# Kernel tuning notes

Hardware: AMD Instinct MI355X
Metric: run time of the kernel (lower is better)

The kernel has to match this reference:

```python
import jax, jax.numpy as jnp
import numpy as np


def _conv3x3_replicate(x, w, b):
    # replicate (edge) padding then VALID 3x3 conv, NCHW / OIHW
    x = jnp.pad(x, ((0, 0), (0, 0), (1, 1), (1, 1)), mode='edge')
    y = jax.lax.conv_general_dilated(
        x, w, window_strides=(1, 1), padding='VALID',
        dimension_numbers=('NCHW', 'OIHW', 'NCHW'))
    return y + b[None, :, None, None]


def setup_inputs() -> dict:
    key = jax.random.key(0)
    ks = jax.random.split(key, 9)
    B, Cin, H, W = 8, 3, 256, 256
    Q, NC, Cout = 64, 32, 64
    x = jax.random.normal(ks[0], (B, Cin, H, W), dtype=jnp.float32)
    # Convx2: two 3x3 convs (replicate padding), then a 1x1 conv
    w1 = jax.random.normal(ks[1], (Q, Cin, 3, 3), dtype=jnp.float32) * (1.0 / np.sqrt(Cin * 9))
    b1 = jnp.zeros((Q,), jnp.float32)
    w2 = jax.random.normal(ks[2], (Q, Q, 3, 3), dtype=jnp.float32) * (1.0 / np.sqrt(Q * 9))
    b2 = jnp.zeros((Q,), jnp.float32)
    w3 = jax.random.normal(ks[3], (Q, Q, 1, 1), dtype=jnp.float32) * (1.0 / np.sqrt(Q))
    b3 = jnp.zeros((Q,), jnp.float32)
    cluster_mu = jax.random.normal(ks[4], (1, NC, Q, 1, 1), dtype=jnp.float32)
    cluster_label = jax.random.normal(ks[5], (Cout, NC), dtype=jnp.float32)
    return {'x': x, 'w1': w1, 'b1': b1, 'w2': w2, 'b2': b2, 'w3': w3, 'b3': b3,
            'cluster_mu': cluster_mu, 'cluster_label': cluster_label}


def reference(x, w1, b1, w2, b2, w3, b3, cluster_mu, cluster_label):
    # query encoder: Convx2 (conv3x3 -> ReLU -> conv3x3 -> ReLU) + 1x1 conv
    q = jax.nn.relu(_conv3x3_replicate(x, w1, b1))
    q = jax.nn.relu(_conv3x3_replicate(q, w2, b2))
    Qd = w3.shape[0]
    q = jnp.einsum('bchw,oc->bohw', q, w3.reshape(Qd, Qd)) + b3[None, :, None, None]  # (B,Q,H,W)
    # squared-distance logits, expanded form: -(||q||^2 - 2 q.mu + ||mu||^2)
    mu = cluster_mu.reshape(cluster_mu.shape[1], cluster_mu.shape[2])  # (NC,Q)
    qn = jnp.sum(q * q, axis=1)                       # (B,H,W)
    dot = jnp.einsum('bqhw,nq->bnhw', q, mu)          # (B,NC,H,W)
    mun = jnp.sum(mu * mu, axis=1)                    # (NC,)
    logit = -(qn[:, None] - 2.0 * dot + mun[None, :, None, None])
    attention = jax.nn.softmax(logit, axis=1)         # (B,NC,H,W)
    res = jnp.einsum('on,bnhw->bohw', cluster_label, attention)
    return res
```

## Files before the change

kernel.cpp:

```cpp
#include <hip/hip_runtime.h>

typedef _Float16 f16x8 __attribute__((ext_vector_type(8)));
typedef __fp16   half2 __attribute__((ext_vector_type(2)));
typedef float    f32x4 __attribute__((ext_vector_type(4)));

#define H_ 256
#define W_ 256

#define WS_W1S 0
#define WS_W2S 4096
#define WS_STG 77824
#define STG_U4 520

#define L_SX   0
#define L_SQ1  4800
#define L_W2S  26304
#define L_STG  63168
#define L_SQ2  26304
#define L_PT   0
#define LDS_SZ 71488

__global__ void repack_kernel(const float* __restrict__ w1, const float* __restrict__ b1,
                              const float* __restrict__ w2, const float* __restrict__ w3,
                              const float* __restrict__ b3, const float* __restrict__ mu,
                              const float* __restrict__ label, char* __restrict__ ws)
{
    int t = blockIdx.x * 256 + threadIdx.x;
    _Float16* w1s  = (_Float16*)(ws + WS_W1S);
    _Float16* w2s  = (_Float16*)(ws + WS_W2S);
    _Float16* mws  = (_Float16*)(ws + WS_STG);
    _Float16* labs = (_Float16*)(ws + WS_STG + 4096);
    float*    tn   = (float*)(ws + WS_STG + 8192);

    if (t < 2048) {
        int o = t >> 5, k = t & 31;
        float v = (k < 27) ? w1[o * 27 + k] : ((k == 27) ? b1[o] : 0.f);
        w1s[o * 32 + k] = (_Float16)v;
    }
    if (t < 36864) {
        int n = t / 576, rem = t % 576, c = rem / 9, tap = rem % 9;
        int chunk = c >> 5, k = c & 31;
        int slot = (k >> 3) ^ ((n ^ (n >> 2)) & 3);
        w2s[((chunk * 9 + tap) * 64 + n) * 32 + slot * 8 + (k & 7)] = (_Float16)w2[t];
    }
    if (t < 2048) {
        int n = t >> 6, c = t & 63;
        float s = 0.f;
        for (int o = 0; o < 64; ++o) s += mu[n * 64 + o] * w3[o * 64 + c];
        int slot = (c >> 3) ^ (n & 7);
        mws[n * 64 + slot * 8 + (c & 7)] = (_Float16)s;
    }
    if (t < 2048) {
        int o = t >> 5, cl = t & 31;
        int slot = (cl >> 3) ^ ((o ^ (o >> 2)) & 3);
        labs[o * 32 + slot * 8 + (cl & 7)] = (_Float16)label[o * 32 + cl];
    }
    if (t < 32) {
        float d = 0.f, m2 = 0.f;
        for (int o = 0; o < 64; ++o) { float m = mu[t * 64 + o]; d += m * b3[o]; m2 += m * m; }
        tn[t] = 2.f * d - m2;
    }
}

__global__ __launch_bounds__(256, 2) void fused_kernel(
    const float* __restrict__ x, const char* __restrict__ ws,
    const float* __restrict__ b2, float* __restrict__ out)
{
    __shared__ __align__(16) char smem[LDS_SZ];
    const int tid = threadIdx.x;
    const int lane = tid & 63;
    const int wv = tid >> 6;
    const int ln = lane & 15;
    const int lg = lane >> 4;
    const int swl = (ln ^ (ln >> 2)) & 3;
    const int w0 = blockIdx.x * 16, h0 = blockIdx.y * 16, bz = blockIdx.z;

    {
        const uint4* s = (const uint4*)(ws + WS_STG);
        uint4* d = (uint4*)(smem + L_STG);
        for (int i = tid; i < STG_U4; i += 256) d[i] = s[i];
    }
    {
        const uint4* s = (const uint4*)(ws + WS_W2S);
        uint4* d = (uint4*)(smem + L_W2S);
        for (int i = tid; i < 2304; i += 256) d[i] = s[i];
    }
    {
        float* sx = (float*)(smem + L_SX);
        for (int i = tid; i < 1200; i += 256) {
            int ci = i / 400, r = (i / 20) % 20, c = i % 20;
            int gy = min(max(h0 - 2 + r, 0), H_ - 1);
            int gx = min(max(w0 - 2 + c, 0), W_ - 1);
            sx[i] = x[((bz * 3 + ci) * H_ + gy) * W_ + gx];
        }
    }
    float b2v[4][4];
#pragma unroll
    for (int nb = 0; nb < 4; ++nb)
#pragma unroll
        for (int jr = 0; jr < 4; ++jr)
            b2v[nb][jr] = b2[nb * 16 + lg * 4 + jr];

    int koff[8]; float kcv[8]; int kvalid[8];
#pragma unroll
    for (int j = 0; j < 8; ++j) {
        int k = lg * 8 + j;
        int ci = (k * 57) >> 9;
        int r  = k - 9 * ci;
        int dy = (r * 22) >> 6;
        int dx = r - 3 * dy;
        koff[j]   = ci * 400 + dy * 20 + dx;
        kvalid[j] = (k < 27);
        kcv[j]    = (k == 27) ? 1.0f : 0.0f;
    }

    __syncthreads();

    const f16x8* w1sp = (const f16x8*)(ws + WS_W1S);
    const float* sxp = (const float*)(smem + L_SX);

    f32x4 acc[4][4];
#pragma unroll
    for (int i = 0; i < 4; ++i)
#pragma unroll
        for (int nb = 0; nb < 4; ++nb)
            acc[i][nb] = (f32x4){b2v[nb][0], b2v[nb][1], b2v[nb][2], b2v[nb][3]};

    f16x8 bfr[6];
    int wrow[6], wswp[6];

    {
        f16x8 w1f[2];
#pragma unroll
        for (int nb2 = 0; nb2 < 2; ++nb2)
            w1f[nb2] = w1sp[(nb2 * 16 + ln) * 4 + lg];
#pragma unroll
        for (int t = 0; t < 6; ++t) {
            int pb = wv + 4 * t;
            if (pb >= 21) break;
            int pos_w = pb * 16 + ln;
            int pos = min(pos_w, 323);
            int sy = (pos * 3641) >> 16;
            int sp = pos - sy * 18;
            int by = min(max(h0 - 1 + sy, 0), H_ - 1) - (h0 - 1);
            int bx = min(max(w0 - 1 + sp, 0), W_ - 1) - (w0 - 1);
            int base = by * 20 + bx;
            float g[8];
#pragma unroll
            for (int j = 0; j < 8; ++j) {
                float v = sxp[base + koff[j]];
                g[j] = kvalid[j] ? v : kcv[j];
            }
            union { half2 h2[4]; f16x8 f; } u;
#pragma unroll
            for (int jj = 0; jj < 4; ++jj)
                u.h2[jj] = __builtin_amdgcn_cvt_pkrtz(g[2 * jj], g[2 * jj + 1]);
            bfr[t] = u.f;
            wrow[t] = pos_w * 64 + ((lg & 1) << 3);
            wswp[t] = (pos_w ^ (pos_w >> 2)) & 3;
#pragma unroll
            for (int nb2 = 0; nb2 < 2; ++nb2) {
                f32x4 c0 = {0.f, 0.f, 0.f, 0.f};
                c0 = __builtin_amdgcn_mfma_f32_16x16x32_f16(w1f[nb2], bfr[t], c0, 0, 0, 0);
                union { half2 h2[2]; uint2 u2; } pk;
                pk.h2[0] = __builtin_amdgcn_cvt_pkrtz(fmaxf(c0[0], 0.f), fmaxf(c0[1], 0.f));
                pk.h2[1] = __builtin_amdgcn_cvt_pkrtz(fmaxf(c0[2], 0.f), fmaxf(c0[3], 0.f));
                int s2 = 2 * nb2 + (lg >> 1);
                *(uint2*)(smem + L_SQ1 + wrow[t] + ((s2 ^ wswp[t]) << 4)) = pk.u2;
            }
        }
    }
    __syncthreads();

#pragma unroll
    for (int tap = 0; tap < 9; ++tap) {
        const int dy = tap / 3, dx = tap % 3;
        f16x8 wf[4], qf[4];
#pragma unroll
        for (int nb = 0; nb < 4; ++nb)
            wf[nb] = *(const f16x8*)(smem + L_W2S + ((tap * 64 + nb * 16 + ln) << 6) + ((lg ^ swl) << 4));
#pragma unroll
        for (int i = 0; i < 4; ++i) {
            int pos = (wv * 4 + i + dy) * 18 + ln + dx;
            int sw = (pos ^ (pos >> 2)) & 3;
            qf[i] = *(const f16x8*)(smem + L_SQ1 + (pos << 6) + ((lg ^ sw) << 4));
        }
#pragma unroll
        for (int i = 0; i < 4; ++i)
#pragma unroll
            for (int nb = 0; nb < 4; ++nb)
                acc[i][nb] = __builtin_amdgcn_mfma_f32_16x16x32_f16(wf[nb], qf[i], acc[i][nb], 0, 0, 0);
    }
    __syncthreads();

    {
        const uint4* s = (const uint4*)(ws + WS_W2S + 36864);
        uint4* d = (uint4*)(smem + L_W2S);
        for (int i = tid; i < 2304; i += 256) d[i] = s[i];
    }
    {
        f16x8 w1f[2];
#pragma unroll
        for (int nb2 = 0; nb2 < 2; ++nb2)
            w1f[nb2] = w1sp[(32 + nb2 * 16 + ln) * 4 + lg];
#pragma unroll
        for (int t = 0; t < 6; ++t) {
            int pb = wv + 4 * t;
            if (pb >= 21) break;
#pragma unroll
            for (int nb2 = 0; nb2 < 2; ++nb2) {
                f32x4 c0 = {0.f, 0.f, 0.f, 0.f};
                c0 = __builtin_amdgcn_mfma_f32_16x16x32_f16(w1f[nb2], bfr[t], c0, 0, 0, 0);
                union { half2 h2[2]; uint2 u2; } pk;
                pk.h2[0] = __builtin_amdgcn_cvt_pkrtz(fmaxf(c0[0], 0.f), fmaxf(c0[1], 0.f));
                pk.h2[1] = __builtin_amdgcn_cvt_pkrtz(fmaxf(c0[2], 0.f), fmaxf(c0[3], 0.f));
                int s2 = 2 * nb2 + (lg >> 1);
                *(uint2*)(smem + L_SQ1 + wrow[t] + ((s2 ^ wswp[t]) << 4)) = pk.u2;
            }
        }
    }
    __syncthreads();

#pragma unroll
    for (int tap = 0; tap < 9; ++tap) {
        const int dy = tap / 3, dx = tap % 3;
        f16x8 wf[4], qf[4];
#pragma unroll
        for (int nb = 0; nb < 4; ++nb)
            wf[nb] = *(const f16x8*)(smem + L_W2S + ((tap * 64 + nb * 16 + ln) << 6) + ((lg ^ swl) << 4));
#pragma unroll
        for (int i = 0; i < 4; ++i) {
            int pos = (wv * 4 + i + dy) * 18 + ln + dx;
            int sw = (pos ^ (pos >> 2)) & 3;
            qf[i] = *(const f16x8*)(smem + L_SQ1 + (pos << 6) + ((lg ^ sw) << 4));
        }
#pragma unroll
        for (int i = 0; i < 4; ++i)
#pragma unroll
            for (int nb = 0; nb < 4; ++nb)
                acc[i][nb] = __builtin_amdgcn_mfma_f32_16x16x32_f16(wf[nb], qf[i], acc[i][nb], 0, 0, 0);
    }
    __syncthreads();

#pragma unroll
    for (int i = 0; i < 4; ++i) {
        int pix = (wv * 4 + i) * 16 + ln;
        int sw = pix & 7;
#pragma unroll
        for (int nb = 0; nb < 4; ++nb) {
            union { half2 h2[2]; uint2 u2; } pk;
            pk.h2[0] = __builtin_amdgcn_cvt_pkrtz(fmaxf(acc[i][nb][0], 0.f), fmaxf(acc[i][nb][1], 0.f));
            pk.h2[1] = __builtin_amdgcn_cvt_pkrtz(fmaxf(acc[i][nb][2], 0.f), fmaxf(acc[i][nb][3], 0.f));
            int s2 = 2 * nb + (lg >> 1);
            *(uint2*)(smem + L_SQ2 + (pix << 7) + ((s2 ^ sw) << 4) + ((lg & 1) << 3)) = pk.u2;
        }
    }
    __syncthreads();

    float tnr[8];
#pragma unroll
    for (int nb2 = 0; nb2 < 2; ++nb2)
#pragma unroll
        for (int jr = 0; jr < 4; ++jr)
            tnr[nb2 * 4 + jr] = *(const float*)(smem + L_STG + 8192 + ((nb2 * 16 + lg * 4 + jr) << 2));

    f32x4 acc3[4][2];
#pragma unroll
    for (int i = 0; i < 4; ++i)
#pragma unroll
        for (int nb2 = 0; nb2 < 2; ++nb2) acc3[i][nb2] = (f32x4){0.f, 0.f, 0.f, 0.f};
#pragma unroll
    for (int ks = 0; ks < 2; ++ks) {
        f16x8 mwf[2], af[4];
#pragma unroll
        for (int nb2 = 0; nb2 < 2; ++nb2)
            mwf[nb2] = *(const f16x8*)(smem + L_STG + ((nb2 * 16 + ln) << 7) + (((ks * 4 + lg) ^ (ln & 7)) << 4));
#pragma unroll
        for (int i = 0; i < 4; ++i) {
            int pix = (wv * 4 + i) * 16 + ln;
            af[i] = *(const f16x8*)(smem + L_SQ2 + (pix << 7) + (((ks * 4 + lg) ^ (pix & 7)) << 4));
        }
#pragma unroll
        for (int i = 0; i < 4; ++i)
#pragma unroll
            for (int nb2 = 0; nb2 < 2; ++nb2)
                acc3[i][nb2] = __builtin_amdgcn_mfma_f32_16x16x32_f16(mwf[nb2], af[i], acc3[i][nb2], 0, 0, 0);
    }

#pragma unroll
    for (int i = 0; i < 4; ++i) {
        float l[8];
#pragma unroll
        for (int nb2 = 0; nb2 < 2; ++nb2)
#pragma unroll
            for (int jr = 0; jr < 4; ++jr)
                l[nb2 * 4 + jr] = 2.f * acc3[i][nb2][jr] + tnr[nb2 * 4 + jr];
        float mx = l[0];
#pragma unroll
        for (int j = 1; j < 8; ++j) mx = fmaxf(mx, l[j]);
        mx = fmaxf(mx, __shfl_xor(mx, 16));
        mx = fmaxf(mx, __shfl_xor(mx, 32));
        float ssum = 0.f;
#pragma unroll
        for (int j = 0; j < 8; ++j) { l[j] = __expf(l[j] - mx); ssum += l[j]; }
        ssum += __shfl_xor(ssum, 16);
        ssum += __shfl_xor(ssum, 32);
        float inv = 1.f / ssum;
        int pix = (wv * 4 + i) * 16 + ln;
        int sw = (pix ^ (pix >> 2)) & 3;
#pragma unroll
        for (int nb2 = 0; nb2 < 2; ++nb2) {
            union { half2 h2[2]; uint2 u2; } pk;
            pk.h2[0] = __builtin_amdgcn_cvt_pkrtz(l[nb2 * 4 + 0] * inv, l[nb2 * 4 + 1] * inv);
            pk.h2[1] = __builtin_amdgcn_cvt_pkrtz(l[nb2 * 4 + 2] * inv, l[nb2 * 4 + 3] * inv);
            int s2 = 2 * nb2 + (lg >> 1);
            *(uint2*)(smem + L_PT + (pix << 6) + ((s2 ^ sw) << 4) + ((lg & 1) << 3)) = pk.u2;
        }
    }
    __syncthreads();

    f16x8 lf[4], pf[4];
#pragma unroll
    for (int nb = 0; nb < 4; ++nb)
        lf[nb] = *(const f16x8*)(smem + L_STG + 4096 + ((nb * 16 + ln) << 6) + ((lg ^ swl) << 4));
#pragma unroll
    for (int i = 0; i < 4; ++i) {
        int pix = (wv * 4 + i) * 16 + ln;
        int sw = (pix ^ (pix >> 2)) & 3;
        pf[i] = *(const f16x8*)(smem + L_PT + (pix << 6) + ((lg ^ sw) << 4));
    }
#pragma unroll
    for (int i = 0; i < 4; ++i) {
        int base = (bz * 64 * H_ + (h0 + wv * 4 + i)) * W_ + w0 + ln;
#pragma unroll
        for (int nb = 0; nb < 4; ++nb) {
            f32x4 c4 = {0.f, 0.f, 0.f, 0.f};
            c4 = __builtin_amdgcn_mfma_f32_16x16x32_f16(lf[nb], pf[i], c4, 0, 0, 0);
#pragma unroll
            for (int jr = 0; jr < 4; ++jr)
                out[base + (nb * 16 + lg * 4 + jr) * (H_ * W_)] = c4[jr];
        }
    }
}

extern "C" void kernel_launch(void* const* d_in, const int* in_sizes, int n_in,
                              void* d_out, int out_size, void* d_ws, size_t ws_size,
                              hipStream_t stream) {
    const float* x  = (const float*)d_in[0];
    const float* w1 = (const float*)d_in[1];
    const float* b1 = (const float*)d_in[2];
    const float* w2 = (const float*)d_in[3];
    const float* b2 = (const float*)d_in[4];
    const float* w3 = (const float*)d_in[5];
    const float* b3 = (const float*)d_in[6];
    const float* mu = (const float*)d_in[7];
    const float* lb = (const float*)d_in[8];
    float* out = (float*)d_out;
    char* ws = (char*)d_ws;

    repack_kernel<<<144, 256, 0, stream>>>(w1, b1, w2, w3, b3, mu, lb, ws);
    dim3 grid(W_ / 16, H_ / 16, 8);
    fused_kernel<<<grid, 256, 0, stream>>>(x, ws, b2, out);
}
```

Before: 82.63 us.

## Read weights directly from global memory and shrink LDS to raise occupancy

Stops staging the conv2 weights, the folded mu/w3 matrix and the labels in shared memory, and has every wave load its MFMA weight fragments straight from the global workspace, which drops the swizzled layout. LDS use falls from about 70 KB to 32 KB and the launch bound goes from 2 to 4 blocks per CU, aiming to hide latency through more waves and to remove the cooperative copy loops. An extra barrier is added before the attention probabilities are written, because the P tile now aliases the SQ2 region at offset 0. The cost is repeated global/L2 loads of the same weights inside the tap loop, and tighter register limits that may cause spills.

New measurement: 184.4 us. 123% more time.

```diff
diff --git a/kernel.cpp b/kernel.cpp
--- a/kernel.cpp
+++ b/kernel.cpp
@@ -10,15 +10,12 @@
 #define WS_W1S 0
 #define WS_W2S 4096
 #define WS_STG 77824
-#define STG_U4 520
 
 #define L_SX   0
 #define L_SQ1  4800
-#define L_W2S  26304
-#define L_STG  63168
-#define L_SQ2  26304
+#define L_SQ2  0
 #define L_PT   0
-#define LDS_SZ 71488
+#define LDS_SZ 32768
 
 __global__ void repack_kernel(const float* __restrict__ w1, const float* __restrict__ b1,
                               const float* __restrict__ w2, const float* __restrict__ w3,
@@ -27,7 +24,7 @@
 {
     int t = blockIdx.x * 256 + threadIdx.x;
     _Float16* w1s  = (_Float16*)(ws + WS_W1S);
-    _Float16* w2s  = (_Float16*)(ws + WS_W2S);
+    _Float16* w2l  = (_Float16*)(ws + WS_W2S);
     _Float16* mws  = (_Float16*)(ws + WS_STG);
     _Float16* labs = (_Float16*)(ws + WS_STG + 4096);
     float*    tn   = (float*)(ws + WS_STG + 8192);
@@ -40,20 +37,17 @@
     if (t < 36864) {
         int n = t / 576, rem = t % 576, c = rem / 9, tap = rem % 9;
         int chunk = c >> 5, k = c & 31;
-        int slot = (k >> 3) ^ ((n ^ (n >> 2)) & 3);
-        w2s[((chunk * 9 + tap) * 64 + n) * 32 + slot * 8 + (k & 7)] = (_Float16)w2[t];
+        w2l[((chunk * 9 + tap) * 64 + n) * 32 + k] = (_Float16)w2[t];
     }
     if (t < 2048) {
         int n = t >> 6, c = t & 63;
         float s = 0.f;
         for (int o = 0; o < 64; ++o) s += mu[n * 64 + o] * w3[o * 64 + c];
-        int slot = (c >> 3) ^ (n & 7);
-        mws[n * 64 + slot * 8 + (c & 7)] = (_Float16)s;
+        mws[n * 64 + c] = (_Float16)s;
     }
     if (t < 2048) {
         int o = t >> 5, cl = t & 31;
-        int slot = (cl >> 3) ^ ((o ^ (o >> 2)) & 3);
-        labs[o * 32 + slot * 8 + (cl & 7)] = (_Float16)label[o * 32 + cl];
+        labs[o * 32 + cl] = (_Float16)label[o * 32 + cl];
     }
     if (t < 32) {
         float d = 0.f, m2 = 0.f;
@@ -62,7 +56,7 @@
     }
 }
 
-__global__ __launch_bounds__(256, 2) void fused_kernel(
+__global__ __launch_bounds__(256, 4) void fused_kernel(
     const float* __restrict__ x, const char* __restrict__ ws,
     const float* __restrict__ b2, float* __restrict__ out)
 {
@@ -72,19 +66,8 @@
     const int wv = tid >> 6;
     const int ln = lane & 15;
     const int lg = lane >> 4;
-    const int swl = (ln ^ (ln >> 2)) & 3;
     const int w0 = blockIdx.x * 16, h0 = blockIdx.y * 16, bz = blockIdx.z;
 
-    {
-        const uint4* s = (const uint4*)(ws + WS_STG);
-        uint4* d = (uint4*)(smem + L_STG);
-        for (int i = tid; i < STG_U4; i += 256) d[i] = s[i];
-    }
-    {
-        const uint4* s = (const uint4*)(ws + WS_W2S);
-        uint4* d = (uint4*)(smem + L_W2S);
-        for (int i = tid; i < 2304; i += 256) d[i] = s[i];
-    }
     {
         float* sx = (float*)(smem + L_SX);
         for (int i = tid; i < 1200; i += 256) {
@@ -178,7 +161,7 @@
         f16x8 wf[4], qf[4];
 #pragma unroll
         for (int nb = 0; nb < 4; ++nb)
-            wf[nb] = *(const f16x8*)(smem + L_W2S + ((tap * 64 + nb * 16 + ln) << 6) + ((lg ^ swl) << 4));
+            wf[nb] = *(const f16x8*)(ws + WS_W2S + ((tap * 64 + nb * 16 + ln) << 6) + (lg << 4));
 #pragma unroll
         for (int i = 0; i < 4; ++i) {
             int pos = (wv * 4 + i + dy) * 18 + ln + dx;
@@ -193,11 +176,6 @@
     }
     __syncthreads();
 
-    {
-        const uint4* s = (const uint4*)(ws + WS_W2S + 36864);
-        uint4* d = (uint4*)(smem + L_W2S);
-        for (int i = tid; i < 2304; i += 256) d[i] = s[i];
-    }
     {
         f16x8 w1f[2];
 #pragma unroll
@@ -227,7 +205,7 @@
         f16x8 wf[4], qf[4];
 #pragma unroll
         for (int nb = 0; nb < 4; ++nb)
-            wf[nb] = *(const f16x8*)(smem + L_W2S + ((tap * 64 + nb * 16 + ln) << 6) + ((lg ^ swl) << 4));
+            wf[nb] = *(const f16x8*)(ws + WS_W2S + 36864 + ((tap * 64 + nb * 16 + ln) << 6) + (lg << 4));
 #pragma unroll
         for (int i = 0; i < 4; ++i) {
             int pos = (wv * 4 + i + dy) * 18 + ln + dx;
@@ -262,7 +240,7 @@
     for (int nb2 = 0; nb2 < 2; ++nb2)
 #pragma unroll
         for (int jr = 0; jr < 4; ++jr)
-            tnr[nb2 * 4 + jr] = *(const float*)(smem + L_STG + 8192 + ((nb2 * 16 + lg * 4 + jr) << 2));
+            tnr[nb2 * 4 + jr] = *(const float*)(ws + WS_STG + 8192 + ((nb2 * 16 + lg * 4 + jr) << 2));
 
     f32x4 acc3[4][2];
 #pragma unroll
@@ -274,7 +252,7 @@
         f16x8 mwf[2], af[4];
 #pragma unroll
         for (int nb2 = 0; nb2 < 2; ++nb2)
-            mwf[nb2] = *(const f16x8*)(smem + L_STG + ((nb2 * 16 + ln) << 7) + (((ks * 4 + lg) ^ (ln & 7)) << 4));
+            mwf[nb2] = *(const f16x8*)(ws + WS_STG + ((nb2 * 16 + ln) << 7) + ((ks * 4 + lg) << 4));
 #pragma unroll
         for (int i = 0; i < 4; ++i) {
             int pix = (wv * 4 + i) * 16 + ln;
@@ -287,6 +265,7 @@
                 acc3[i][nb2] = __builtin_amdgcn_mfma_f32_16x16x32_f16(mwf[nb2], af[i], acc3[i][nb2], 0, 0, 0);
     }
 
+    float pv[4][8];
 #pragma unroll
     for (int i = 0; i < 4; ++i) {
         float l[8];
@@ -306,13 +285,20 @@
         ssum += __shfl_xor(ssum, 16);
         ssum += __shfl_xor(ssum, 32);
         float inv = 1.f / ssum;
+#pragma unroll
+        for (int j = 0; j < 8; ++j) pv[i][j] = l[j] * inv;
+    }
+    __syncthreads();
+
+#pragma unroll
+    for (int i = 0; i < 4; ++i) {
         int pix = (wv * 4 + i) * 16 + ln;
         int sw = (pix ^ (pix >> 2)) & 3;
 #pragma unroll
         for (int nb2 = 0; nb2 < 2; ++nb2) {
             union { half2 h2[2]; uint2 u2; } pk;
-            pk.h2[0] = __builtin_amdgcn_cvt_pkrtz(l[nb2 * 4 + 0] * inv, l[nb2 * 4 + 1] * inv);
-            pk.h2[1] = __builtin_amdgcn_cvt_pkrtz(l[nb2 * 4 + 2] * inv, l[nb2 * 4 + 3] * inv);
+            pk.h2[0] = __builtin_amdgcn_cvt_pkrtz(pv[i][nb2 * 4 + 0], pv[i][nb2 * 4 + 1]);
+            pk.h2[1] = __builtin_amdgcn_cvt_pkrtz(pv[i][nb2 * 4 + 2], pv[i][nb2 * 4 + 3]);
             int s2 = 2 * nb2 + (lg >> 1);
             *(uint2*)(smem + L_PT + (pix << 6) + ((s2 ^ sw) << 4) + ((lg & 1) << 3)) = pk.u2;
         }
@@ -322,7 +308,7 @@
     f16x8 lf[4], pf[4];
 #pragma unroll
     for (int nb = 0; nb < 4; ++nb)
-        lf[nb] = *(const f16x8*)(smem + L_STG + 4096 + ((nb * 16 + ln) << 6) + ((lg ^ swl) << 4));
+        lf[nb] = *(const f16x8*)(ws + WS_STG + 4096 + ((nb * 16 + ln) << 6) + (lg << 4));
 #pragma unroll
     for (int i = 0; i < 4; ++i) {
         int pix = (wv * 4 + i) * 16 + ln;
```
